# Performance work log

Measured on AMD Instinct MI355X. Metric: run time of the kernel, lower is better.

The kernel has to match this reference:

```python
import jax, jax.numpy as jnp
import numpy as np

N_HEADS = 16


def apply_rotary_emb(x, cos, sin):
    # x: [B, H, S, hd]; cos/sin: [S, hd//2] (broadcast over B, H)
    xr = x.reshape(x.shape[:-1] + (-1, 2))
    r, i = xr[..., 0], xr[..., 1]
    a = r * cos - i * sin
    b = i * cos + r * sin
    return jnp.stack([a, b], axis=-1).reshape(x.shape).astype(x.dtype)


def setup_inputs() -> dict:
    key = jax.random.key(0)
    ks = jax.random.split(key, 7)
    B, S, D = 2, 2048, 1024
    hd = D // N_HEADS
    x = jax.random.normal(ks[0], (B, S, D), dtype=jnp.float32)
    freqs_cos = jax.random.uniform(ks[1], (S, hd // 2), dtype=jnp.float32)
    freqs_sin = jax.random.uniform(ks[2], (S, hd // 2), dtype=jnp.float32)
    sc = 1.0 / np.sqrt(D)
    Wq = jax.random.normal(ks[3], (D, D), dtype=jnp.float32) * sc
    Wk = jax.random.normal(ks[4], (D, D), dtype=jnp.float32) * sc
    Wv = jax.random.normal(ks[5], (D, D), dtype=jnp.float32) * sc
    Wo = jax.random.normal(ks[6], (D, D), dtype=jnp.float32) * sc
    return {"x": x, "freqs_cos": freqs_cos, "freqs_sin": freqs_sin,
            "Wq": Wq, "Wk": Wk, "Wv": Wv, "Wo": Wo}


def reference(x, freqs_cos, freqs_sin, Wq, Wk, Wv, Wo):
    B, S, D = x.shape
    H = N_HEADS
    hd = D // H
    # QKV projections (nn.Linear: x @ W.T)
    q = (x @ Wq.T).reshape(B, S, H, hd).transpose(0, 2, 1, 3)
    k = (x @ Wk.T).reshape(B, S, H, hd).transpose(0, 2, 1, 3)
    v = (x @ Wv.T).reshape(B, S, H, hd).transpose(0, 2, 1, 3)
    q = apply_rotary_emb(q, freqs_cos, freqs_sin)
    k = apply_rotary_emb(k, freqs_cos, freqs_sin)
    # causal SDPA (scale = 1/sqrt(head_dim), as in F.scaled_dot_product_attention)
    scores = jnp.einsum("bhqd,bhkd->bhqk", q, k) * (1.0 / np.sqrt(hd))
    causal = jnp.tril(jnp.ones((S, S), dtype=bool))
    scores = jnp.where(causal, scores, -jnp.inf)
    probs = jax.nn.softmax(scores, axis=-1)
    attn_out = jnp.einsum("bhqk,bhkd->bhqd", probs, v)
    attn_cat = attn_out.transpose(0, 2, 1, 3).reshape(B, S, D)
    return attn_cat @ Wo.T
```

## Files before the change

### kernel.cpp

```cpp
#include <hip/hip_runtime.h>
#include <hip/hip_bf16.h>
#include <cstdint>

typedef __attribute__((ext_vector_type(8))) short short8;
typedef __attribute__((ext_vector_type(4))) float f32x4;

#define B_  2
#define S_  2048
#define D_  1024
#define H_  16
#define HD  64

static __device__ __forceinline__ float bf2f(unsigned int u16) {
    union { unsigned int i; float f; } v; v.i = u16 << 16; return v.f;
}
static __device__ __forceinline__ unsigned short f2bf(float f) {
    union { float f; unsigned int i; } v; v.f = f;
    unsigned int r = v.i + 0x7FFFu + ((v.i >> 16) & 1u);
    return (unsigned short)(r >> 16);
}
static __device__ __forceinline__ unsigned pack_bf16(float hi, float lo) {
    union { float f; unsigned u; } h, l;
    h.f = hi; l.f = lo;
    return __builtin_amdgcn_perm(h.u + 0x8000u, l.u + 0x8000u, 0x07060302);
}
static __device__ __forceinline__ void load_lds_16B(const unsigned short* g, unsigned short* l) {
    __builtin_amdgcn_global_load_lds(
        (const __attribute__((address_space(1))) unsigned int*)g,
        (__attribute__((address_space(3))) unsigned int*)l, 16, 0, 0);
}

__global__ void cvt_all(const float* __restrict__ x,
                        const float* __restrict__ w0, const float* __restrict__ w1,
                        const float* __restrict__ w2, const float* __restrict__ w3,
                        unsigned short* __restrict__ xbf,
                        unsigned short* __restrict__ wdst) {
    int bid = blockIdx.x;
    if (bid < 4096) {
        int i = bid * 256 + threadIdx.x;
        float4 f = ((const float4*)x)[i];
        uint2 o;
        o.x = (unsigned int)f2bf(f.x) | ((unsigned int)f2bf(f.y) << 16);
        o.y = (unsigned int)f2bf(f.z) | ((unsigned int)f2bf(f.w) << 16);
        ((uint2*)xbf)[i] = o;
    } else {
        int wb = bid - 4096;
        int wsel = wb >> 10;
        const float* s = wsel == 0 ? w0 : wsel == 1 ? w1 : wsel == 2 ? w2 : w3;
        int i = (wb & 1023) * 256 + threadIdx.x;
        float4 f = ((const float4*)s)[i];
        uint2 o;
        o.x = (unsigned int)f2bf(f.x) | ((unsigned int)f2bf(f.y) << 16);
        o.y = (unsigned int)f2bf(f.z) | ((unsigned int)f2bf(f.w) << 16);
        ((uint2*)wdst)[(size_t)wsel * 262144 + i] = o;
    }
}

__global__ __launch_bounds__(256) void qkv_gemm(
    const unsigned short* __restrict__ xbf,
    const unsigned short* __restrict__ wq,
    const unsigned short* __restrict__ wk,
    const unsigned short* __restrict__ wv,
    const float* __restrict__ fcos,
    const float* __restrict__ fsin,
    unsigned short* __restrict__ qb,
    unsigned short* __restrict__ kb,
    unsigned short* __restrict__ vb)
{
    __shared__ unsigned short As[128 * 32];
    __shared__ unsigned short Bs[128 * 32];
    __shared__ unsigned short Tt[64][136];

    const int tid  = threadIdx.x;
    const int w    = tid >> 6, lane = tid & 63;
    const int l15  = lane & 15, quad = lane >> 4;
    const int wrow = (w >> 1) * 64, wcol = (w & 1) * 64;

    const int m0 = blockIdx.x * 128;
    const int nc = blockIdx.y * 128;
    const int sel = nc >> 10;
    const int n0 = nc & 1023;
    const unsigned short* __restrict__ W = sel == 0 ? wq : (sel == 1 ? wk : wv);

    const int lr = lane >> 2, lc = (lane & 3) * 8;
    const unsigned short* ga = xbf + (size_t)(m0 + w * 16 + lr) * 1024 + lc;
    const unsigned short* gb = W   + (size_t)(n0 + w * 16 + lr) * 1024 + lc;
    unsigned short* la0 = As + (w * 16) * 32;
    unsigned short* la1 = As + (64 + w * 16) * 32;
    unsigned short* lb0 = Bs + (w * 16) * 32;
    unsigned short* lb1 = Bs + (64 + w * 16) * 32;

    f32x4 acc[4][4] = {};

    for (int k0 = 0; k0 < 1024; k0 += 32) {
        __syncthreads();
        load_lds_16B(ga + k0,             la0);
        load_lds_16B(ga + 64 * 1024 + k0, la1);
        load_lds_16B(gb + k0,             lb0);
        load_lds_16B(gb + 64 * 1024 + k0, lb1);
        __syncthreads();

        short8 a[4], b[4];
#pragma unroll
        for (int i = 0; i < 4; i++)
            a[i] = *(const short8*)&As[(wrow + i * 16 + l15) * 32 + quad * 8];
#pragma unroll
        for (int j = 0; j < 4; j++)
            b[j] = *(const short8*)&Bs[(wcol + j * 16 + l15) * 32 + quad * 8];
#pragma unroll
        for (int i = 0; i < 4; i++)
#pragma unroll
            for (int j = 0; j < 4; j++)
                acc[i][j] = __builtin_amdgcn_mfma_f32_16x16x32_bf16(a[i], b[j], acc[i][j], 0, 0, 0);
    }

    if (sel == 2) {
        const int bb  = blockIdx.x >> 4;
        const int m0s = (blockIdx.x & 15) * 128;
        const int h0  = n0 >> 6;
        const int nh  = w & 1;
#pragma unroll
        for (int half = 0; half < 2; half++) {
            __syncthreads();
            if (nh == half) {
#pragma unroll
                for (int i = 0; i < 4; i++)
#pragma unroll
                    for (int j = 0; j < 4; j++) {
                        uint2 pk;
                        pk.x = pack_bf16(acc[i][j][1], acc[i][j][0]);
                        pk.y = pack_bf16(acc[i][j][3], acc[i][j][2]);
                        *(uint2*)&Tt[j * 16 + l15][wrow + i * 16 + quad * 4] = pk;
                    }
            }
            __syncthreads();
            const int row = tid >> 2, cq = tid & 3;
            unsigned short* vrow = vb +
                (((size_t)(bb * H_ + h0 + half)) * HD + row) * S_ + m0s + cq * 32;
#pragma unroll
            for (int k = 0; k < 4; k++) {
                short8 v = *(const short8*)&Tt[row][cq * 32 + k * 8];
                *(short8*)(vrow + k * 8) = v;
            }
        }
    } else {
        unsigned short* __restrict__ Out = sel == 0 ? qb : kb;
        const float qsc = (sel == 0) ? 0.125f * 1.44269504f : 1.0f;
        const int odd = l15 & 1;
#pragma unroll
        for (int i = 0; i < 4; i++)
#pragma unroll
            for (int r = 0; r < 4; r++) {
                int m = m0 + wrow + i * 16 + quad * 4 + r;
                int bb = m >> 11, s = m & 2047;
#pragma unroll
                for (int j = 0; j < 4; j++) {
                    int n = n0 + wcol + j * 16 + l15;
                    int h = n >> 6, d = n & 63;
                    int t = d >> 1;
                    float c  = fcos[s * 32 + t];
                    float si = fsin[s * 32 + t];
                    float own = acc[i][j][r];
                    float oth = __shfl_xor(own, 1, 64);
                    float outv = odd ? (own * c + oth * si) : (own * c - oth * si);
                    Out[(((size_t)(bb * H_ + h) * S_) + s) * HD + d] = f2bf(outv * qsc);
                }
            }
    }
}

__global__ __launch_bounds__(256) void out_gemm(
    const unsigned short* __restrict__ A,
    const unsigned short* __restrict__ Bt,
    float* __restrict__ C)
{
    __shared__ unsigned short As[128 * 32];
    __shared__ unsigned short Bs[64 * 32];

    const int tid  = threadIdx.x;
    const int w    = tid >> 6, lane = tid & 63;
    const int l15  = lane & 15, quad = lane >> 4;
    const int wrow = (w >> 1) * 64, wcol = (w & 1) * 32;

    const int m0 = blockIdx.x * 128;
    const int n0 = blockIdx.y * 64;

    const int lr = lane >> 2, lc = (lane & 3) * 8;
    const unsigned short* ga = A  + (size_t)(m0 + w * 16 + lr) * 1024 + lc;
    const unsigned short* gb = Bt + (size_t)(n0 + w * 16 + lr) * 1024 + lc;
    unsigned short* la0 = As + (w * 16) * 32;
    unsigned short* la1 = As + (64 + w * 16) * 32;
    unsigned short* lb0 = Bs + (w * 16) * 32;

    f32x4 acc[4][2] = {};

    for (int k0 = 0; k0 < 1024; k0 += 32) {
        __syncthreads();
        load_lds_16B(ga + k0,             la0);
        load_lds_16B(ga + 64 * 1024 + k0, la1);
        load_lds_16B(gb + k0,             lb0);
        __syncthreads();

        short8 a[4], b[2];
#pragma unroll
        for (int i = 0; i < 4; i++)
            a[i] = *(const short8*)&As[(wrow + i * 16 + l15) * 32 + quad * 8];
#pragma unroll
        for (int j = 0; j < 2; j++)
            b[j] = *(const short8*)&Bs[(wcol + j * 16 + l15) * 32 + quad * 8];
#pragma unroll
        for (int i = 0; i < 4; i++)
#pragma unroll
            for (int j = 0; j < 2; j++)
                acc[i][j] = __builtin_amdgcn_mfma_f32_16x16x32_bf16(a[i], b[j], acc[i][j], 0, 0, 0);
    }

#pragma unroll
    for (int i = 0; i < 4; i++)
#pragma unroll
        for (int r = 0; r < 4; r++) {
            int m = m0 + wrow + i * 16 + quad * 4 + r;
#pragma unroll
            for (int j = 0; j < 2; j++)
                C[(size_t)m * 1024 + n0 + wcol + j * 16 + l15] = acc[i][j][r];
        }
}

__global__ __launch_bounds__(256) void flash_attn_mfma(
    const unsigned short* __restrict__ qb,
    const unsigned short* __restrict__ kb,
    const unsigned short* __restrict__ vT,
    unsigned short* __restrict__ attnc)
{
    __shared__ __attribute__((aligned(1024))) unsigned short Ks[2][2][64][32];
    __shared__ __attribute__((aligned(1024))) unsigned short Vt[64][64];
    __shared__ unsigned short Pls[4][16][72];

    const int bh   = blockIdx.x;
    const int qtb  = blockIdx.y;
    const int jj = qtb & 7, mm = qtb >> 3;
    const int qt = (mm == 0) ? jj : (mm == 1) ? 31 - jj : (mm == 2) ? 8 + jj : 23 - jj;

    const int b    = bh >> 4, h = bh & 15;
    const int tid  = threadIdx.x;
    const int w    = tid >> 6;
    const int lane = tid & 63;
    const int l15  = lane & 15;
    const int quad = lane >> 4;

    const size_t bhS = (size_t)bh * S_;
    const unsigned short* __restrict__ vTb = vT + (size_t)bh * HD * S_;

    short8 qfrag[2];
    {
        const unsigned short* qp = qb + (bhS + qt * 64 + w * 16 + l15) * HD + quad * 8;
        qfrag[0] = *(const short8*)(qp);
        qfrag[1] = *(const short8*)(qp + 32);
    }

    const int ksrow  = lane >> 2;
    const int ksslot = (lane & 3) ^ ((lane >> 3) & 3);
    const int vsrow  = lane >> 3;
    const int vsslot = (lane & 7) ^ vsrow;

    const int ckq = (quad ^ ((l15 >> 1) & 3)) << 4;
    const int s7  = l15 & 7;

    short8 ones;
#pragma unroll
    for (int i = 0; i < 8; i++) ones[i] = (short)0x3F80;

    f32x4 O[4] = {};
    f32x4 Osum = {};
    float mrow = -INFINITY;

    auto STAGE_K = [&](int jt, int bufi) {
        const int j0 = jt * 64;
        const unsigned short* kg = kb + (bhS + j0 + w * 16 + ksrow) * HD + ksslot * 8;
        load_lds_16B(kg,      &Ks[bufi][0][w * 16][0]);
        load_lds_16B(kg + 32, &Ks[bufi][1][w * 16][0]);
    };
    auto STAGE_V = [&](int jt) {
        const int j0 = jt * 64;
        const unsigned short* vg = vTb + (size_t)(w * 16 + vsrow) * S_ + j0 + vsslot * 8;
        load_lds_16B(vg,          &Vt[w * 16][0]);
        load_lds_16B(vg + 8 * S_, &Vt[w * 16 + 8][0]);
    };

    STAGE_K(0, 0);

    for (int jt = 0; jt <= qt; jt++) {
        const int cur = jt & 1;
        if (jt < qt) {
            STAGE_K(jt + 1, cur ^ 1);
            STAGE_V(jt);
            asm volatile("s_waitcnt vmcnt(4)" ::: "memory");
        } else {
            STAGE_V(jt);
            asm volatile("s_waitcnt vmcnt(2)" ::: "memory");
        }
        __builtin_amdgcn_s_barrier();

        const bool diag  = (jt == qt);
        const int  nsub  = diag ? (w + 1) : 4;
        const int  kgmax = (nsub + 1) >> 1;

        f32x4 Sacc[4];
        float tmax = -INFINITY;
        for (int sub = 0; sub < nsub; sub++) {
            f32x4 s = {};
#pragma unroll
            for (int kh = 0; kh < 2; kh++) {
                int bo = ((sub * 16 + l15) << 6) + ckq;
                short8 kf = *(const short8*)((const char*)&Ks[cur][kh][0][0] + bo);
                s = __builtin_amdgcn_mfma_f32_16x16x32_bf16(kf, qfrag[kh], s, 0, 0, 0);
            }
#pragma unroll
            for (int r = 0; r < 4; r++) {
                float v = s[r];
                if (diag && (sub * 16 + quad * 4 + r > w * 16 + l15)) v = -INFINITY;
                s[r] = v;
                tmax = fmaxf(tmax, v);
            }
            Sacc[sub] = s;
        }
        tmax = fmaxf(tmax, __shfl_xor(tmax, 16, 64));
        tmax = fmaxf(tmax, __shfl_xor(tmax, 32, 64));

        if (__any(tmax > mrow + 8.0f)) {
            float mnew = fmaxf(mrow, tmax);
            float ccr  = __builtin_amdgcn_exp2f(mrow - mnew);
#pragma unroll
            for (int r = 0; r < 4; r++) {
                float ccq = __shfl(ccr, quad * 4 + r, 64);
#pragma unroll
                for (int dt = 0; dt < 4; dt++) O[dt][r] *= ccq;
                Osum[r] *= ccq;
            }
            mrow = mnew;
        }

        for (int sub = 0; sub < nsub; sub++) {
            f32x4 s = Sacc[sub];
            float p0 = __builtin_amdgcn_exp2f(s[0] - mrow);
            float p1 = __builtin_amdgcn_exp2f(s[1] - mrow);
            float p2 = __builtin_amdgcn_exp2f(s[2] - mrow);
            float p3 = __builtin_amdgcn_exp2f(s[3] - mrow);
            uint2 pk;
            pk.x = pack_bf16(p1, p0);
            pk.y = pack_bf16(p3, p2);
            *(uint2*)&Pls[w][l15][sub * 16 + quad * 4] = pk;
        }
        if (diag) {
            for (int sub = nsub; sub < 2 * kgmax; sub++) {
                uint2 z; z.x = 0u; z.y = 0u;
                *(uint2*)&Pls[w][l15][sub * 16 + quad * 4] = z;
            }
        }

        if (jt < qt) {
            asm volatile("s_waitcnt vmcnt(2)" ::: "memory");
        } else {
            asm volatile("s_waitcnt vmcnt(0)" ::: "memory");
        }
        __builtin_amdgcn_s_barrier();

        for (int kg = 0; kg < kgmax; kg++) {
            short8 pf = *(const short8*)&Pls[w][l15][kg * 32 + quad * 8];
#pragma unroll
            for (int dt = 0; dt < 4; dt++) {
                int row = dt * 16 + l15;
                int slot = (((kg << 2) | quad) ^ s7) << 4;
                short8 vf = *(const short8*)((const char*)&Vt[0][0] + (row << 7) + slot);
                O[dt] = __builtin_amdgcn_mfma_f32_16x16x32_bf16(pf, vf, O[dt], 0, 0, 0);
            }
            Osum = __builtin_amdgcn_mfma_f32_16x16x32_bf16(pf, ones, Osum, 0, 0, 0);
        }

        asm volatile("" ::: "memory");
        __builtin_amdgcn_s_barrier();
    }

#pragma unroll
    for (int r = 0; r < 4; r++) {
        float invq = 1.0f / Osum[r];
        int qabs = qt * 64 + w * 16 + quad * 4 + r;
        unsigned short* op = attnc + (((size_t)b * S_ + qabs) * H_ + h) * HD + l15;
#pragma unroll
        for (int dt = 0; dt < 4; dt++)
            op[dt * 16] = f2bf(O[dt][r] * invq);
    }
}

extern "C" void kernel_launch(void* const* d_in, const int* in_sizes, int n_in,
                              void* d_out, int out_size, void* d_ws, size_t ws_size,
                              hipStream_t stream) {
    const float* x    = (const float*)d_in[0];
    const float* fcos = (const float*)d_in[1];
    const float* fsin = (const float*)d_in[2];
    const float* Wq   = (const float*)d_in[3];
    const float* Wk   = (const float*)d_in[4];
    const float* Wv   = (const float*)d_in[5];
    const float* Wo   = (const float*)d_in[6];
    float* out = (float*)d_out;

    unsigned short* ws = (unsigned short*)d_ws;
    unsigned short* xbf = ws;
    unsigned short* wqb = xbf + 4096 * 1024;
    unsigned short* wkb = wqb + 1024 * 1024;
    unsigned short* wvb = wkb + 1024 * 1024;
    unsigned short* wob = wvb + 1024 * 1024;
    unsigned short* qb  = wob + 1024 * 1024;
    unsigned short* kb  = qb + 4096 * 1024;
    unsigned short* vb  = kb + 4096 * 1024;
    unsigned short* attnc = vb + 4096 * 1024;

    cvt_all<<<8192, 256, 0, stream>>>(x, Wq, Wk, Wv, Wo, xbf, wqb);

    qkv_gemm<<<dim3(32, 24), 256, 0, stream>>>(xbf, wqb, wkb, wvb, fcos, fsin, qb, kb, vb);

    flash_attn_mfma<<<dim3(32, 32), 256, 0, stream>>>(qb, kb, vb, attnc);

    out_gemm<<<dim3(32, 16), 256, 0, stream>>>(attnc, wob, out);
}
```

Before: 216.2 us.

## Double-buffer LDS tiles in QKV and output projection GEMMs

Converts the K-loop of both projection GEMMs to a two-stage LDS ping-pong, issuing the global-to-LDS loads for the next K tile before computing on the current one. This cuts the barriers per iteration from two to one and lets memory traffic overlap with MFMA work. The QKV kernel now reuses the first buffer as the transpose scratch for the V epilogue. It doubles the LDS footprint of the output GEMM, and correctness depends on the load_lds_16B completion semantics being covered by the single barrier.

```diff
diff --git a/kernel.cpp b/kernel.cpp
--- a/kernel.cpp
+++ b/kernel.cpp
@@ -67,9 +67,7 @@
     unsigned short* __restrict__ kb,
     unsigned short* __restrict__ vb)
 {
-    __shared__ unsigned short As[128 * 32];
-    __shared__ unsigned short Bs[128 * 32];
-    __shared__ unsigned short Tt[64][136];
+    __shared__ unsigned short pool[2][2][128 * 32];
 
     const int tid  = threadIdx.x;
     const int w    = tid >> 6, lane = tid & 63;
@@ -85,36 +83,42 @@
     const int lr = lane >> 2, lc = (lane & 3) * 8;
     const unsigned short* ga = xbf + (size_t)(m0 + w * 16 + lr) * 1024 + lc;
     const unsigned short* gb = W   + (size_t)(n0 + w * 16 + lr) * 1024 + lc;
-    unsigned short* la0 = As + (w * 16) * 32;
-    unsigned short* la1 = As + (64 + w * 16) * 32;
-    unsigned short* lb0 = Bs + (w * 16) * 32;
-    unsigned short* lb1 = Bs + (64 + w * 16) * 32;
 
     f32x4 acc[4][4] = {};
 
+    auto STAGE = [&](int k0, int bufi) {
+        load_lds_16B(ga + k0,             &pool[bufi][0][(w * 16) * 32]);
+        load_lds_16B(ga + 64 * 1024 + k0, &pool[bufi][0][(64 + w * 16) * 32]);
+        load_lds_16B(gb + k0,             &pool[bufi][1][(w * 16) * 32]);
+        load_lds_16B(gb + 64 * 1024 + k0, &pool[bufi][1][(64 + w * 16) * 32]);
+    };
+
+    STAGE(0, 0);
+    __syncthreads();
+
+    int cur = 0;
     for (int k0 = 0; k0 < 1024; k0 += 32) {
-        __syncthreads();
-        load_lds_16B(ga + k0,             la0);
-        load_lds_16B(ga + 64 * 1024 + k0, la1);
-        load_lds_16B(gb + k0,             lb0);
-        load_lds_16B(gb + 64 * 1024 + k0, lb1);
-        __syncthreads();
+        if (k0 + 32 < 1024) STAGE(k0 + 32, cur ^ 1);
 
         short8 a[4], b[4];
 #pragma unroll
         for (int i = 0; i < 4; i++)
-            a[i] = *(const short8*)&As[(wrow + i * 16 + l15) * 32 + quad * 8];
+            a[i] = *(const short8*)&pool[cur][0][(wrow + i * 16 + l15) * 32 + quad * 8];
 #pragma unroll
         for (int j = 0; j < 4; j++)
-            b[j] = *(const short8*)&Bs[(wcol + j * 16 + l15) * 32 + quad * 8];
+            b[j] = *(const short8*)&pool[cur][1][(wcol + j * 16 + l15) * 32 + quad * 8];
 #pragma unroll
         for (int i = 0; i < 4; i++)
 #pragma unroll
             for (int j = 0; j < 4; j++)
                 acc[i][j] = __builtin_amdgcn_mfma_f32_16x16x32_bf16(a[i], b[j], acc[i][j], 0, 0, 0);
+
+        __syncthreads();
+        cur ^= 1;
     }
 
     if (sel == 2) {
+        unsigned short (*Tt)[136] = reinterpret_cast<unsigned short (*)[136]>(&pool[0][0][0]);
         const int bb  = blockIdx.x >> 4;
         const int m0s = (blockIdx.x & 15) * 128;
         const int h0  = n0 >> 6;
@@ -174,8 +178,8 @@
     const unsigned short* __restrict__ Bt,
     float* __restrict__ C)
 {
-    __shared__ unsigned short As[128 * 32];
-    __shared__ unsigned short Bs[64 * 32];
+    __shared__ unsigned short Apool[2][128 * 32];
+    __shared__ unsigned short Bpool[2][64 * 32];
 
     const int tid  = threadIdx.x;
     const int w    = tid >> 6, lane = tid & 63;
@@ -188,31 +192,37 @@
     const int lr = lane >> 2, lc = (lane & 3) * 8;
     const unsigned short* ga = A  + (size_t)(m0 + w * 16 + lr) * 1024 + lc;
     const unsigned short* gb = Bt + (size_t)(n0 + w * 16 + lr) * 1024 + lc;
-    unsigned short* la0 = As + (w * 16) * 32;
-    unsigned short* la1 = As + (64 + w * 16) * 32;
-    unsigned short* lb0 = Bs + (w * 16) * 32;
 
     f32x4 acc[4][2] = {};
 
+    auto STAGE = [&](int k0, int bufi) {
+        load_lds_16B(ga + k0,             &Apool[bufi][(w * 16) * 32]);
+        load_lds_16B(ga + 64 * 1024 + k0, &Apool[bufi][(64 + w * 16) * 32]);
+        load_lds_16B(gb + k0,             &Bpool[bufi][(w * 16) * 32]);
+    };
+
+    STAGE(0, 0);
+    __syncthreads();
+
+    int cur = 0;
     for (int k0 = 0; k0 < 1024; k0 += 32) {
-        __syncthreads();
-        load_lds_16B(ga + k0,             la0);
-        load_lds_16B(ga + 64 * 1024 + k0, la1);
-        load_lds_16B(gb + k0,             lb0);
-        __syncthreads();
+        if (k0 + 32 < 1024) STAGE(k0 + 32, cur ^ 1);
 
         short8 a[4], b[2];
 #pragma unroll
         for (int i = 0; i < 4; i++)
-            a[i] = *(const short8*)&As[(wrow + i * 16 + l15) * 32 + quad * 8];
+            a[i] = *(const short8*)&Apool[cur][(wrow + i * 16 + l15) * 32 + quad * 8];
 #pragma unroll
         for (int j = 0; j < 2; j++)
-            b[j] = *(const short8*)&Bs[(wcol + j * 16 + l15) * 32 + quad * 8];
+            b[j] = *(const short8*)&Bpool[cur][(wcol + j * 16 + l15) * 32 + quad * 8];
 #pragma unroll
         for (int i = 0; i < 4; i++)
 #pragma unroll
             for (int j = 0; j < 2; j++)
                 acc[i][j] = __builtin_amdgcn_mfma_f32_16x16x32_bf16(a[i], b[j], acc[i][j], 0, 0, 0);
+
+        __syncthreads();
+        cur ^= 1;
     }
 
 #pragma unroll
```

Result: faster. 210.8 us (-2.5%).
